# Optimization experiments

Measured on AMD Instinct MI355X. Metric: run time of the kernel, lower is better.

Reference implementation:

```python
import jax, jax.numpy as jnp
import numpy as np

TAU = 2.0      # spikingjelly LIFNode default tau
V_TH = 1.0     # default v_threshold
ALPHA = 4.0    # default surrogate.Sigmoid alpha


@jax.custom_vjp
def spike_fn(v):
    # Heaviside(v - v_th) with sigmoid surrogate gradient
    return (v >= V_TH).astype(v.dtype)

def _spike_fwd(v):
    return (v >= V_TH).astype(v.dtype), v

def _spike_bwd(v, g):
    s = jax.nn.sigmoid(ALPHA * (v - V_TH))
    return (g * ALPHA * s * (1.0 - s),)

spike_fn.defvjp(_spike_fwd, _spike_bwd)


def lif(x):
    """Multi-step LIF: decay_input=False, hard reset to v_reset=0, detach_reset.
    x: [T, B, C, N] -> spikes [T, B, C, N]."""
    def step(v, xt):
        v = v * (1.0 - 1.0 / TAU) + xt          # v = v - (v - 0)/tau + x
        s = spike_fn(v)
        v = v * (1.0 - jax.lax.stop_gradient(s))  # hard reset, detached spike
        return v, s
    v0 = jnp.zeros_like(x[0])
    _, spikes = jax.lax.scan(step, v0, x)
    return spikes


def setup_inputs() -> dict:
    key = jax.random.key(0)
    kx, k1, k2, k3 = jax.random.split(key, 4)
    T, B, C, dim = 4, 32, 196, 768
    scale = dim ** -0.5
    x = jax.random.normal(kx, (T, B, C, dim), dtype=jnp.float32)
    w1 = jax.random.normal(k1, (dim, dim), dtype=jnp.float32) * scale
    w2 = jax.random.normal(k2, (dim, dim), dtype=jnp.float32) * scale
    w3 = jax.random.normal(k3, (dim, dim), dtype=jnp.float32) * scale
    return {"x": x, "w1": w1, "w2": w2, "w3": w3}


def reference(x, w1, w2, w3):
    # y1 = mlp1(mlp1_lif(x)); y2 = mlp2(mlp2_lif(x)); out = mlp3(y1 * mlp3_lif(y2))
    y1 = jnp.einsum('tbcn,mn->tbcm', lif(x), w1)
    y2 = jnp.einsum('tbcn,mn->tbcm', lif(x), w2)
    out = jnp.einsum('tbcn,mn->tbcm', y1 * lif(y2), w3)
    return out
```

## Files before the change

### kernel.cpp

```cpp
#include <hip/hip_runtime.h>
#include <stdint.h>

#define T_STEPS 4
#define BC      6272
#define NDIM    768
#define TBC     (T_STEPS*BC)
#define BCN     (BC*NDIM)
#define FIX_CAP 65536

typedef unsigned short u16;
typedef __attribute__((ext_vector_type(8))) __bf16 bf16x8;
typedef __attribute__((ext_vector_type(4))) float f32x4;
typedef __attribute__((ext_vector_type(4))) int   i32x4;

#define MFMA16(a,b,c)  __builtin_amdgcn_mfma_f32_16x16x32_bf16((a),(b),(c),0,0,0)
#define MFMAI8(a,b,c)  __builtin_amdgcn_mfma_i32_16x16x64_i8((a),(b),(c),0,0,0)

__device__ __forceinline__ u16 f2b(float f) {
    uint32_t u = __builtin_bit_cast(uint32_t, f);
    u += 0x7FFFu + ((u >> 16) & 1u);
    return (u16)(u >> 16);
}
__device__ __forceinline__ void gload16(const void* g, void* l) {
    __builtin_amdgcn_global_load_lds((const __attribute__((address_space(1))) void*)g,
                                     (__attribute__((address_space(3))) void*)l,
                                     16, 0, 0);
}

__global__ __launch_bounds__(256) void front_kernel(
    const float* __restrict__ x,
    const float* __restrict__ w1, const float* __restrict__ w2,
    const float* __restrict__ w3,
    int8_t* __restrict__ s8, u16* __restrict__ cnt,
    int8_t* __restrict__ w1q, int8_t* __restrict__ w2h,
    int8_t* __restrict__ w2l, u16* __restrict__ w3b,
    uint32_t* __restrict__ fix_cnt)
{
    if (blockIdx.x < BC / 4) {
        const int bc   = blockIdx.x * 4 + (threadIdx.x >> 6);
        const int lane = threadIdx.x & 63;
        const size_t base = (size_t)bc * NDIM + lane * 12;

        double v[12];
        #pragma unroll
        for (int j = 0; j < 12; ++j) v[j] = 0.0;
        uint32_t c01 = 0, c23 = 0;

        #pragma unroll
        for (int t = 0; t < T_STEPS; ++t) {
            float4 xa = *(const float4*)&x[(size_t)t * BCN + base + 0];
            float4 xb = *(const float4*)&x[(size_t)t * BCN + base + 4];
            float4 xc = *(const float4*)&x[(size_t)t * BCN + base + 8];
            float xs[12] = {xa.x, xa.y, xa.z, xa.w, xb.x, xb.y, xb.z, xb.w,
                            xc.x, xc.y, xc.z, xc.w};
            uint32_t pk[3] = {0, 0, 0};
            uint32_t csum = 0;
            #pragma unroll
            for (int j = 0; j < 12; ++j) {
                v[j] = 0.5 * v[j] + (double)xs[j];
                if (v[j] >= 1.0) {
                    pk[j >> 2] |= 1u << ((j & 3) * 8);
                    csum++;
                    v[j] = 0.0;
                }
            }
            uint32_t* dst = (uint32_t*)&s8[(size_t)t * BCN + base];
            dst[0] = pk[0]; dst[1] = pk[1]; dst[2] = pk[2];
            if (t < 2) c01 += csum << (t * 16);
            else       c23 += csum << ((t - 2) * 16);
        }
        #pragma unroll
        for (int o = 32; o > 0; o >>= 1) {
            c01 += __shfl_xor(c01, o);
            c23 += __shfl_xor(c23, o);
        }
        if (lane == 0) {
            cnt[0 * BC + bc] = (u16)(c01 & 0xFFFF);
            cnt[1 * BC + bc] = (u16)(c01 >> 16);
            cnt[2 * BC + bc] = (u16)(c23 & 0xFFFF);
            cnt[3 * BC + bc] = (u16)(c23 >> 16);
        }
    } else {
        int i = (blockIdx.x - BC / 4) * 256 + threadIdx.x;
        if (i == 0) *fix_cnt = 0;
        int q1 = __float2int_rn(w1[i] * 512.0f);
        q1 = q1 > 127 ? 127 : (q1 < -127 ? -127 : q1);
        w1q[i] = (int8_t)q1;
        int q16 = __double2int_rn((double)w2[i] * 65536.0);
        int8_t lo = (int8_t)(q16 & 0xFF);
        int hi = (q16 - (int)lo) >> 8;
        w2h[i] = (int8_t)hi;
        w2l[i] = lo;
        w3b[i] = f2b(w3[i]);
    }
}

__global__ __launch_bounds__(256, 3) void y12_kernel(
    const int8_t* __restrict__ s8,
    const int8_t* __restrict__ w1q, const int8_t* __restrict__ w2hb,
    const int8_t* __restrict__ w2lb,
    const u16* __restrict__ cnt,
    u16* __restrict__ z,
    uint32_t* __restrict__ fix_cnt,
    int2* __restrict__ fix_idx, float4* __restrict__ fix_y1)
{
    __shared__ int8_t lds[2][16384];

    const int lane = threadIdx.x & 63;
    const int wid  = threadIdx.x >> 6;

    const int bid = blockIdx.x;
    const int swz = (bid & 7) * 588 + (bid >> 3);
    const int mb  = swz % (NDIM / 64);
    const int rb  = swz / (NDIM / 64);
    const int m0  = mb * 64;
    const int bc0 = rb * 16;

    const int srow  = lane >> 2;
    const int scolB = ((lane & 3) ^ ((lane >> 3) & 3)) << 4;
    const int8_t* gp[4];
    int lofs[4];
    #pragma unroll
    for (int c = 0; c < 4; ++c) {
        int chunk = wid * 4 + c;
        const int8_t* g;
        int l;
        if (chunk < 4) {
            int gr = chunk * 16 + srow;
            int t = gr >> 4, bcl = gr & 15;
            g = s8 + ((size_t)(t * BC + bc0 + bcl)) * NDIM + scolB;
            l = chunk * 1024;
        } else if (chunk < 8) {
            int mr = (chunk - 4) * 16 + srow;
            g = w1q + ((size_t)(m0 + mr)) * NDIM + scolB;
            l = 4096 + (chunk - 4) * 1024;
        } else if (chunk < 12) {
            int mr = (chunk - 8) * 16 + srow;
            g = w2hb + ((size_t)(m0 + mr)) * NDIM + scolB;
            l = 8192 + (chunk - 8) * 1024;
        } else {
            int mr = (chunk - 12) * 16 + srow;
            g = w2lb + ((size_t)(m0 + mr)) * NDIM + scolB;
            l = 12288 + (chunk - 12) * 1024;
        }
        gp[c] = g;
        lofs[c] = l;
    }

    const int slotb = (((lane >> 4) ^ ((lane >> 1) & 3)) << 4);
    int aoff[4];
    #pragma unroll
    for (int t = 0; t < 4; ++t)
        aoff[t] = (t * 16 + (lane & 15)) * 64 + slotb;
    const int boff = (wid * 16 + (lane & 15)) * 64 + slotb;

    i32x4 a1[4], ah[4], al[4];
    #pragma unroll
    for (int t = 0; t < 4; ++t) {
        a1[t] = (i32x4){0, 0, 0, 0};
        ah[t] = (i32x4){0, 0, 0, 0};
        al[t] = (i32x4){0, 0, 0, 0};
    }

    auto stage = [&](int buf) {
        #pragma unroll
        for (int c = 0; c < 4; ++c) {
            gload16(gp[c], &lds[buf][lofs[c]]);
            gp[c] += 64;
        }
    };
    auto compute = [&](int buf) {
        const int8_t* L = lds[buf];
        i32x4 b1 = *(const i32x4*)&L[ 4096 + boff];
        i32x4 bh = *(const i32x4*)&L[ 8192 + boff];
        i32x4 bl = *(const i32x4*)&L[12288 + boff];
        #pragma unroll
        for (int t = 0; t < 4; ++t) {
            i32x4 a = *(const i32x4*)&L[aoff[t]];
            a1[t] = MFMAI8(a, b1, a1[t]);
            ah[t] = MFMAI8(a, bh, ah[t]);
            al[t] = MFMAI8(a, bl, al[t]);
        }
    };

    stage(0);
    __syncthreads();
    for (int it = 0; it < 11; ++it) {
        stage((it + 1) & 1);
        compute(it & 1);
        __syncthreads();
    }
    compute(1);

    const int mg = m0 + wid * 16 + (lane & 15);
    #pragma unroll
    for (int r = 0; r < 4; ++r) {
        const int bcg = bc0 + (lane >> 4) * 4 + r;
        double v = 0.0, e = 0.0;
        bool flag = false;
        float zv[4], y1v[4];
        #pragma unroll
        for (int t = 0; t < 4; ++t) {
            float y1 = (float)a1[t][r] * (1.0f / 512.0f);
            y1v[t] = y1;
            double y2 = (double)(ah[t][r] * 256 + al[t][r]) * (1.0 / 65536.0);
            v = 0.5 * v + y2;
            e = 0.5 * e + 7.62939453125e-6 * (double)cnt[t * BC + bcg] + 1e-9;
            double d = v - 1.0;
            flag |= (d <= e && d >= -e);
            if (v >= 1.0) { zv[t] = y1; v = 0.0; e = 0.0; }
            else          { zv[t] = 0.0f; }
        }
        if (flag) {
            uint32_t id = atomicAdd(fix_cnt, 1u);
            if (id < FIX_CAP) {
                fix_idx[id] = make_int2(bcg, mg);
                fix_y1[id]  = make_float4(y1v[0], y1v[1], y1v[2], y1v[3]);
            }
        }
        #pragma unroll
        for (int t = 0; t < 4; ++t)
            z[((size_t)(t * BC + bcg)) * NDIM + mg] = f2b(zv[t]);
    }
}

__global__ __launch_bounds__(256) void fixup_kernel(
    const int8_t* __restrict__ s8, const float* __restrict__ w2,
    const int2* __restrict__ fix_idx, const float4* __restrict__ fix_y1,
    const uint32_t* __restrict__ fix_cnt, u16* __restrict__ z)
{
    const int lane = threadIdx.x & 63;
    const int wave = (blockIdx.x * 256 + threadIdx.x) >> 6;
    const int nw   = gridDim.x * 4;
    uint32_t n = *fix_cnt;
    if (n > FIX_CAP) n = FIX_CAP;

    for (uint32_t e = wave; e < n; e += nw) {
        const int bc = fix_idx[e].x, m = fix_idx[e].y;
        const float* w2row = w2 + (size_t)m * NDIM;
        double acc[4] = {0.0, 0.0, 0.0, 0.0};
        #pragma unroll
        for (int j = 0; j < NDIM / 64; ++j) {
            int nn = lane + j * 64;
            double wv = (double)w2row[nn];
            #pragma unroll
            for (int t = 0; t < 4; ++t)
                if (s8[((size_t)(t * BC + bc)) * NDIM + nn]) acc[t] += wv;
        }
        #pragma unroll
        for (int o = 32; o > 0; o >>= 1)
            #pragma unroll
            for (int t = 0; t < 4; ++t) acc[t] += __shfl_xor(acc[t], o);
        if (lane == 0) {
            float4 y1 = fix_y1[e];
            float y1a[4] = {y1.x, y1.y, y1.z, y1.w};
            double v = 0.0;
            #pragma unroll
            for (int t = 0; t < 4; ++t) {
                v = 0.5 * v + acc[t];
                u16 zz = 0;
                if (v >= 1.0) { zz = f2b(y1a[t]); v = 0.0; }
                z[((size_t)(t * BC + bc)) * NDIM + m] = zz;
            }
        }
    }
}

__global__ __launch_bounds__(256, 2) void out_kernel(
    const u16* __restrict__ z, const u16* __restrict__ w3b,
    float* __restrict__ out)
{
    __shared__ u16 lds[2][16384];

    const int lane = threadIdx.x & 63;
    const int wid  = threadIdx.x >> 6;
    const int rw   = wid >> 1;
    const int cw   = wid & 1;

    const int bid = blockIdx.x;
    const int swz = (bid & 7) * 147 + (bid >> 3);
    const int mb  = swz % (NDIM / 128);
    const int rb  = swz / (NDIM / 128);
    const int m0  = mb * 128;
    const int r0  = rb * 128;

    const int srow  = lane >> 3;
    const int scolE = ((((lane & 7) << 4) ^ ((srow & 7) << 4)) >> 1);
    const u16* gp[8];
    int lofs[8];
    #pragma unroll
    for (int c = 0; c < 8; ++c) {
        int chunk = wid * 8 + c;
        const u16* g;
        if (chunk < 16) {
            int gr = chunk * 8 + srow;
            g = z + ((size_t)(r0 + gr)) * NDIM + scolE;
        } else {
            int mr = (chunk - 16) * 8 + srow;
            g = w3b + ((size_t)(m0 + mr)) * NDIM + scolE;
        }
        gp[c] = g;
        lofs[c] = chunk * 512;
    }

    const int swzb = (lane & 7) << 4;
    const int cb   = (lane >> 4) << 4;
    const int colE0 = ((cb     ) ^ swzb) >> 1;
    const int colE1 = ((cb | 64) ^ swzb) >> 1;

    f32x4 acc[4][4];
    #pragma unroll
    for (int rt = 0; rt < 4; ++rt)
        #pragma unroll
        for (int cf = 0; cf < 4; ++cf) acc[rt][cf] = (f32x4){0.f, 0.f, 0.f, 0.f};

    auto stage = [&](int buf) {
        #pragma unroll
        for (int c = 0; c < 8; ++c) {
            gload16(gp[c], &lds[buf][lofs[c]]);
            gp[c] += 64;
        }
    };
    auto compute = [&](int buf) {
        const u16* L = lds[buf];
        #pragma unroll
        for (int k2i = 0; k2i < 2; ++k2i) {
            const int ce = k2i ? colE1 : colE0;
            bf16x8 bw[4];
            #pragma unroll
            for (int cf = 0; cf < 4; ++cf)
                bw[cf] = *(const bf16x8*)&L[8192 + (cw * 64 + cf * 16 + (lane & 15)) * 64 + ce];
            #pragma unroll
            for (int rt = 0; rt < 4; ++rt) {
                bf16x8 az = *(const bf16x8*)&L[(rw * 64 + rt * 16 + (lane & 15)) * 64 + ce];
                #pragma unroll
                for (int cf = 0; cf < 4; ++cf)
                    acc[rt][cf] = MFMA16(az, bw[cf], acc[rt][cf]);
            }
        }
    };

    stage(0);
    __syncthreads();
    for (int it = 0; it < 11; ++it) {
        stage((it + 1) & 1);
        compute(it & 1);
        __syncthreads();
    }
    compute(1);

    #pragma unroll
    for (int rt = 0; rt < 4; ++rt)
        #pragma unroll
        for (int cf = 0; cf < 4; ++cf)
            #pragma unroll
            for (int r = 0; r < 4; ++r)
                out[((size_t)(r0 + rw * 64 + rt * 16 + (lane >> 4) * 4 + r)) * NDIM
                    + m0 + cw * 64 + cf * 16 + (lane & 15)] = acc[rt][cf][r];
}

extern "C" void kernel_launch(void* const* d_in, const int* in_sizes, int n_in,
                              void* d_out, int out_size, void* d_ws, size_t ws_size,
                              hipStream_t stream) {
    const float* x  = (const float*)d_in[0];
    const float* w1 = (const float*)d_in[1];
    const float* w2 = (const float*)d_in[2];
    const float* w3 = (const float*)d_in[3];
    float* out = (float*)d_out;

    char* ws = (char*)d_ws;
    int8_t*   s8      = (int8_t*)(ws);
    u16*      z       = (u16*)(ws + 19267584);
    int8_t*   w1q     = (int8_t*)(ws + 57802752);
    int8_t*   w2h     = (int8_t*)(ws + 58392576);
    int8_t*   w2l     = (int8_t*)(ws + 58982400);
    u16*      w3b     = (u16*)(ws + 59572224);
    u16*      cnt     = (u16*)(ws + 60751872);
    uint32_t* fix_cnt = (uint32_t*)(ws + 60802048);
    int2*     fix_idx = (int2*)(ws + 60802112);
    float4*   fix_y1  = (float4*)(ws + 61326400);

    front_kernel<<<BC / 4 + (NDIM * NDIM) / 256, 256, 0, stream>>>(
        x, w1, w2, w3, s8, cnt, w1q, w2h, w2l, w3b, fix_cnt);
    y12_kernel<<<(BC / 16) * (NDIM / 64), 256, 0, stream>>>(s8, w1q, w2h, w2l,
                                                            cnt, z, fix_cnt,
                                                            fix_idx, fix_y1);
    fixup_kernel<<<128, 256, 0, stream>>>(s8, w2, fix_idx, fix_y1, fix_cnt, z);
    out_kernel<<<(TBC / 128) * (NDIM / 128), 256, 0, stream>>>(z, w3b, out);
}
```

Measured before the change: 142.7 us.

## Enlarge y12 tile to 32x128 using 32x32x32 int8 MFMA

Result: slower. 150.0 us (+5.1%).

```diff
diff --git a/kernel.cpp b/kernel.cpp
--- a/kernel.cpp
+++ b/kernel.cpp
@@ -10,11 +10,12 @@
 
 typedef unsigned short u16;
 typedef __attribute__((ext_vector_type(8))) __bf16 bf16x8;
-typedef __attribute__((ext_vector_type(4))) float f32x4;
-typedef __attribute__((ext_vector_type(4))) int   i32x4;
-
-#define MFMA16(a,b,c)  __builtin_amdgcn_mfma_f32_16x16x32_bf16((a),(b),(c),0,0,0)
-#define MFMAI8(a,b,c)  __builtin_amdgcn_mfma_i32_16x16x64_i8((a),(b),(c),0,0,0)
+typedef __attribute__((ext_vector_type(4)))  float f32x4;
+typedef __attribute__((ext_vector_type(4)))  int   i32x4;
+typedef __attribute__((ext_vector_type(16))) int   i32x16;
+
+#define MFMA16(a,b,c)   __builtin_amdgcn_mfma_f32_16x16x32_bf16((a),(b),(c),0,0,0)
+#define MFMAI8_32(a,b,c) __builtin_amdgcn_mfma_i32_32x32x32_i8((a),(b),(c),0,0,0)
 
 __device__ __forceinline__ u16 f2b(float f) {
     uint32_t u = __builtin_bit_cast(uint32_t, f);
@@ -95,7 +96,7 @@
     }
 }
 
-__global__ __launch_bounds__(256, 3) void y12_kernel(
+__global__ __launch_bounds__(256) void y12_kernel(
     const int8_t* __restrict__ s8,
     const int8_t* __restrict__ w1q, const int8_t* __restrict__ w2hb,
     const int8_t* __restrict__ w2lb,
@@ -104,82 +105,86 @@
     uint32_t* __restrict__ fix_cnt,
     int2* __restrict__ fix_idx, float4* __restrict__ fix_y1)
 {
-    __shared__ int8_t lds[2][16384];
+    __shared__ int8_t lds[2][32768];
 
     const int lane = threadIdx.x & 63;
     const int wid  = threadIdx.x >> 6;
 
     const int bid = blockIdx.x;
-    const int swz = (bid & 7) * 588 + (bid >> 3);
-    const int mb  = swz % (NDIM / 64);
-    const int rb  = swz / (NDIM / 64);
-    const int m0  = mb * 64;
-    const int bc0 = rb * 16;
+    const int swz = (bid & 7) * 147 + (bid >> 3);
+    const int mb  = swz % (NDIM / 128);
+    const int rb  = swz / (NDIM / 128);
+    const int m0  = mb * 128;
+    const int bc0 = rb * 32;
 
     const int srow  = lane >> 2;
-    const int scolB = ((lane & 3) ^ ((lane >> 3) & 3)) << 4;
-    const int8_t* gp[4];
-    int lofs[4];
-    #pragma unroll
-    for (int c = 0; c < 4; ++c) {
-        int chunk = wid * 4 + c;
+    const int scolB = ((lane & 3) ^ ((lane >> 2) & 3)) << 4;
+    const int8_t* gp[8];
+    int lofs[8];
+    #pragma unroll
+    for (int c = 0; c < 8; ++c) {
+        int chunk = wid * 8 + c;
         const int8_t* g;
         int l;
-        if (chunk < 4) {
+        if (chunk < 8) {
             int gr = chunk * 16 + srow;
-            int t = gr >> 4, bcl = gr & 15;
+            int t = gr >> 5, bcl = gr & 31;
             g = s8 + ((size_t)(t * BC + bc0 + bcl)) * NDIM + scolB;
             l = chunk * 1024;
-        } else if (chunk < 8) {
-            int mr = (chunk - 4) * 16 + srow;
+        } else if (chunk < 16) {
+            int mr = (chunk - 8) * 16 + srow;
             g = w1q + ((size_t)(m0 + mr)) * NDIM + scolB;
-            l = 4096 + (chunk - 4) * 1024;
-        } else if (chunk < 12) {
-            int mr = (chunk - 8) * 16 + srow;
+            l = 8192 + (chunk - 8) * 1024;
+        } else if (chunk < 24) {
+            int mr = (chunk - 16) * 16 + srow;
             g = w2hb + ((size_t)(m0 + mr)) * NDIM + scolB;
-            l = 8192 + (chunk - 8) * 1024;
+            l = 16384 + (chunk - 16) * 1024;
         } else {
-            int mr = (chunk - 12) * 16 + srow;
+            int mr = (chunk - 24) * 16 + srow;
             g = w2lb + ((size_t)(m0 + mr)) * NDIM + scolB;
-            l = 12288 + (chunk - 12) * 1024;
+            l = 24576 + (chunk - 24) * 1024;
         }
         gp[c] = g;
         lofs[c] = l;
     }
 
-    const int slotb = (((lane >> 4) ^ ((lane >> 1) & 3)) << 4);
-    int aoff[4];
-    #pragma unroll
-    for (int t = 0; t < 4; ++t)
-        aoff[t] = (t * 16 + (lane & 15)) * 64 + slotb;
-    const int boff = (wid * 16 + (lane & 15)) * 64 + slotb;
-
-    i32x4 a1[4], ah[4], al[4];
+    const int rloc = lane & 31;
+    const int half = lane >> 5;
+    const int sl0  = ((half      ^ (lane & 3)) << 4);
+    const int sl1  = (((2 | half) ^ (lane & 3)) << 4);
+    const int arow = rloc * 64;
+    const int brow = (wid * 32 + rloc) * 64;
+
+    i32x16 a1[4], ah[4], al[4];
     #pragma unroll
     for (int t = 0; t < 4; ++t) {
-        a1[t] = (i32x4){0, 0, 0, 0};
-        ah[t] = (i32x4){0, 0, 0, 0};
-        al[t] = (i32x4){0, 0, 0, 0};
+        a1[t] = (i32x16)(0);
+        ah[t] = (i32x16)(0);
+        al[t] = (i32x16)(0);
     }
 
     auto stage = [&](int buf) {
         #pragma unroll
-        for (int c = 0; c < 4; ++c) {
+        for (int c = 0; c < 8; ++c) {
             gload16(gp[c], &lds[buf][lofs[c]]);
             gp[c] += 64;
         }
     };
     auto compute = [&](int buf) {
         const int8_t* L = lds[buf];
-        i32x4 b1 = *(const i32x4*)&L[ 4096 + boff];
-        i32x4 bh = *(const i32x4*)&L[ 8192 + boff];
-        i32x4 bl = *(const i32x4*)&L[12288 + boff];
-        #pragma unroll
-        for (int t = 0; t < 4; ++t) {
-            i32x4 a = *(const i32x4*)&L[aoff[t]];
-            a1[t] = MFMAI8(a, b1, a1[t]);
-            ah[t] = MFMAI8(a, bh, ah[t]);
-            al[t] = MFMAI8(a, bl, al[t]);
+        #pragma unroll
+        for (int ks = 0; ks < 2; ++ks) {
+            const int sl = ks ? sl1 : sl0;
+            i32x4 b1 = *(const i32x4*)&L[ 8192 + brow + sl];
+            i32x4 bh = *(const i32x4*)&L[16384 + brow + sl];
+            i32x4 bl = *(const i32x4*)&L[24576 + brow + sl];
+            #pragma unroll
+            for (int t = 0; t < 4; ++t) {
+                i32x4 a = *(const i32x4*)&L[arow + t * 2048 + sl];
+                a1[t] = MFMAI8_32(a, b1, a1[t]);
+                ah[t] = MFMAI8_32(a, bh, ah[t]);
+                al[t] = MFMAI8_32(a, bl, al[t]);
+            }
         }
     };
 
@@ -192,10 +197,10 @@
     }
     compute(1);
 
-    const int mg = m0 + wid * 16 + (lane & 15);
-    #pragma unroll
-    for (int r = 0; r < 4; ++r) {
-        const int bcg = bc0 + (lane >> 4) * 4 + r;
+    const int mg = m0 + wid * 32 + rloc;
+    #pragma unroll
+    for (int r = 0; r < 16; ++r) {
+        const int bcg = bc0 + (r & 3) + ((r >> 2) << 3) + (half << 2);
         double v = 0.0, e = 0.0;
         bool flag = false;
         float zv[4], y1v[4];
@@ -382,9 +387,9 @@
 
     front_kernel<<<BC / 4 + (NDIM * NDIM) / 256, 256, 0, stream>>>(
         x, w1, w2, w3, s8, cnt, w1q, w2h, w2l, w3b, fix_cnt);
-    y12_kernel<<<(BC / 16) * (NDIM / 64), 256, 0, stream>>>(s8, w1q, w2h, w2l,
-                                                            cnt, z, fix_cnt,
-                                                            fix_idx, fix_y1);
-    fixup_kernel<<<128, 256, 0, stream>>>(s8, w2, fix_idx, fix_y1, fix_cnt, z);
+    y12_kernel<<<(BC / 32) * (NDIM / 128), 256, 0, stream>>>(s8, w1q, w2h, w2l,
+                                                             cnt, z, fix_cnt,
+                                                             fix_idx, fix_y1);
+    fixup_kernel<<<512, 256, 0, stream>>>(s8, w2, fix_idx, fix_y1, fix_cnt, z);
     out_kernel<<<(TBC / 128) * (NDIM / 128), 256, 0, stream>>>(z, w3b, out);
 }
```
